# Kernel tuning notes

Measured on AMD Instinct MI355X. Metric: run time of the kernel, lower is better.

## Reference

```python
import jax, jax.numpy as jnp
import numpy as np

D_MODEL = 1024
EXPAND = 2
D_INNER = D_MODEL * EXPAND  # 2048
D_CONV = 4
B, T = 4, 4096
LN_EPS = 1e-5


def setup_inputs() -> dict:
    key = jax.random.key(0)
    ks = jax.random.split(key, 6)
    x = jax.random.normal(ks[0], (B, T, D_MODEL), dtype=jnp.float32)
    gamma = jnp.ones((D_MODEL,), jnp.float32)
    beta = jnp.zeros((D_MODEL,), jnp.float32)
    # in_proj: Linear(d_model -> 2*d_inner, bias=False); torch weight [out,in]
    W_in = jax.random.normal(ks[1], (2 * D_INNER, D_MODEL), jnp.float32) / np.sqrt(D_MODEL)
    # depthwise conv1d: weight [d_inner, 1, d_conv], bias [d_inner]
    conv_w = jax.random.normal(ks[2], (D_INNER, 1, D_CONV), jnp.float32) / np.sqrt(D_CONV)
    conv_b = jax.random.normal(ks[3], (D_INNER,), jnp.float32) * 0.01
    # out_proj: Linear(d_inner -> d_model, bias=False)
    W_out = jax.random.normal(ks[4], (D_MODEL, D_INNER), jnp.float32) / np.sqrt(D_INNER)
    return {"x": x, "gamma": gamma, "beta": beta, "W_in": W_in,
            "conv_w": conv_w, "conv_b": conv_b, "W_out": W_out}


def _silu(v):
    return v * jax.nn.sigmoid(v)


def reference(x, gamma, beta, W_in, conv_w, conv_b, W_out):
    residual = x
    # LayerNorm
    mu = jnp.mean(x, axis=-1, keepdims=True)
    var = jnp.mean(jnp.square(x - mu), axis=-1, keepdims=True)
    xn = (x - mu) * jax.lax.rsqrt(var + LN_EPS) * gamma + beta
    # in_proj -> split gate
    xz = jnp.einsum('btd,ed->bte', xn, W_in)  # [B,T,2*D_INNER]
    x_part, z = jnp.split(xz, 2, axis=-1)
    # causal depthwise conv: torch pads both sides by d_conv-1 then slices [:T]
    # == left pad (d_conv-1), no right pad
    lhs = jnp.transpose(x_part, (0, 2, 1))  # [B, D_INNER, T]
    x_conv = jax.lax.conv_general_dilated(
        lhs, conv_w, window_strides=(1,), padding=[(D_CONV - 1, 0)],
        feature_group_count=D_INNER,
        dimension_numbers=('NCH', 'OIH', 'NCH')) + conv_b[None, :, None]
    x_conv = jnp.transpose(x_conv, (0, 2, 1))  # [B,T,D_INNER]
    y = _silu(x_conv) * _silu(z)
    out = jnp.einsum('bte,de->btd', y, W_out)
    return residual + out  # dropout=0 (eval) -> identity
```

## Files before the change

### kernel.cpp

```cpp
#include <hip/hip_runtime.h>
#include <hip/hip_bf16.h>

#define D_MODEL 1024
#define D_INNER 2048
#define NTOK    16384
#define TLEN    4096
#define LN_EPS  1e-5f

typedef unsigned short u16;
typedef unsigned short u16x4 __attribute__((ext_vector_type(4)));
typedef unsigned short u16x8 __attribute__((ext_vector_type(8)));
typedef __bf16        bf16x8 __attribute__((ext_vector_type(8)));
typedef float         f32x4  __attribute__((ext_vector_type(4)));

__device__ __forceinline__ float b2f(u16 u) {
    union { float f; unsigned int i; } v; v.i = ((unsigned int)u) << 16; return v.f;
}
__device__ __forceinline__ u16 f2b(float f) {
    union { float f; unsigned int i; } v; v.f = f;
    unsigned int r = v.i + 0x7fffu + ((v.i >> 16) & 1u);
    return (u16)(r >> 16);
}

__device__ __forceinline__ void gld_lds16(const u16* g, u16* l) {
    __builtin_amdgcn_global_load_lds(
        (const __attribute__((address_space(1))) void*)g,
        (__attribute__((address_space(3))) void*)l, 16, 0, 0);
}

__device__ __forceinline__ void ln_body(
    int row, int tid,
    const float* __restrict__ x, const float* __restrict__ gamma,
    const float* __restrict__ beta, u16* __restrict__ xn)
{
    const float* xr = x + (size_t)row * D_MODEL;
    const int c0 = tid * 4;

    f32x4 xv = *(const f32x4*)(xr + c0);
    float s = 0.f, s2 = 0.f;
#pragma unroll
    for (int i = 0; i < 4; i++) { s += xv[i]; s2 += xv[i] * xv[i]; }

#pragma unroll
    for (int off = 32; off > 0; off >>= 1) {
        s  += __shfl_down(s,  off);
        s2 += __shfl_down(s2, off);
    }
    __shared__ float red[8];
    const int wave = tid >> 6, lane = tid & 63;
    if (lane == 0) { red[wave] = s; red[4 + wave] = s2; }
    __syncthreads();
    const float ts  = red[0] + red[1] + red[2] + red[3];
    const float ts2 = red[4] + red[5] + red[6] + red[7];
    const float mu  = ts * (1.0f / D_MODEL);
    const float var = ts2 * (1.0f / D_MODEL) - mu * mu;
    const float inv = rsqrtf(var + LN_EPS);

    f32x4 gv = *(const f32x4*)(gamma + c0);
    f32x4 bv = *(const f32x4*)(beta + c0);
    u16x4 out;
#pragma unroll
    for (int i = 0; i < 4; i++)
        out[i] = f2b((xv[i] - mu) * inv * gv[i] + bv[i]);
    *(u16x4*)(xn + (size_t)row * D_MODEL + c0) = out;
}

__global__ __launch_bounds__(256) void prep_kernel(
    const float* __restrict__ x, const float* __restrict__ gamma,
    const float* __restrict__ beta, u16* __restrict__ xn,
    const float* __restrict__ W_in, u16* __restrict__ wbin,
    const float* __restrict__ W_out, u16* __restrict__ wbout,
    const float* __restrict__ conv_w, float* __restrict__ wt,
    int lnRows)
{
    const int b   = blockIdx.x;
    const int tid = threadIdx.x;

    if (b < lnRows) {
        ln_body(b, tid, x, gamma, beta, xn);
        return;
    }
    int rb = b - lnRows;
    if (rb < 4096) {
        const int o = (rb * 256 + tid) * 4;
        f32x4 v = *(const f32x4*)(W_in + o);
        u16x4 w;
#pragma unroll
        for (int j = 0; j < 4; j++) w[j] = f2b(v[j]);
        *(u16x4*)(wbin + o) = w;
        return;
    }
    rb -= 4096;
    if (rb < 2048) {
        const int o = (rb * 256 + tid) * 4;
        f32x4 v = *(const f32x4*)(W_out + o);
        u16x4 w;
#pragma unroll
        for (int j = 0; j < 4; j++) w[j] = f2b(v[j]);
        *(u16x4*)(wbout + o) = w;
        return;
    }
    rb -= 2048;
    const int i = rb * 256 + tid;
    const int ch = i >> 2, j = i & 3;
    wt[j * D_INNER + ch] = conv_w[i];
}

__global__ __launch_bounds__(256) void ln_kernel(
    const float* __restrict__ x, const float* __restrict__ gamma,
    const float* __restrict__ beta, u16* __restrict__ xn)
{
    ln_body(blockIdx.x, threadIdx.x, x, gamma, beta, xn);
}

#define BAR()      __builtin_amdgcn_s_barrier()
#define WAIT_VM6() asm volatile("s_waitcnt vmcnt(6)" ::: "memory")
#define WAIT_VM0() asm volatile("s_waitcnt vmcnt(0)" ::: "memory")

#define STAGE_A(ldsb, s0, s1, kt) do { \
    gld_lds16(Ag + (size_t)(s0) * K + (kt) + goff, &(ldsb)[(s0) * 64]); \
    gld_lds16(Ag + (size_t)(s1) * K + (kt) + goff, &(ldsb)[(s1) * 64]); \
} while (0)
#define STAGE_B(ldsb, s0, s1, kt) do { \
    gld_lds16(Bg + (size_t)(s0) * K + (kt) + goff, &(ldsb)[(s0) * 64]); \
    gld_lds16(Bg + (size_t)(s1) * K + (kt) + goff, &(ldsb)[(s1) * 64]); \
} while (0)

#define RD_A(base, roff) do { \
    _Pragma("unroll") for (int m_ = 0; m_ < 4; m_++) { \
        const u16* p_ = (base) + (arow0 + (roff) + m_ * 16) * 64; \
        aF[m_][0] = __builtin_bit_cast(bf16x8, *(const u16x8*)(p_ + cx0)); \
        aF[m_][1] = __builtin_bit_cast(bf16x8, *(const u16x8*)(p_ + cx1)); \
    } } while (0)
#define RD_B(base, dst, roff) do { \
    _Pragma("unroll") for (int n_ = 0; n_ < 2; n_++) { \
        const u16* p_ = (base) + (brow0 + (roff) + n_ * 16) * 64; \
        dst[n_][0] = __builtin_bit_cast(bf16x8, *(const u16x8*)(p_ + cx0)); \
        dst[n_][1] = __builtin_bit_cast(bf16x8, *(const u16x8*)(p_ + cx1)); \
    } } while (0)

#define MMA_Q(m0, n0, BB) do { \
    _Pragma("unroll") for (int m_ = 0; m_ < 4; m_++) \
    _Pragma("unroll") for (int n_ = 0; n_ < 2; n_++) \
    _Pragma("unroll") for (int k_ = 0; k_ < 2; k_++) \
        acc[(m0) + m_][(n0) + n_] = __builtin_amdgcn_mfma_f32_16x16x32_bf16( \
            aF[m_][k_], BB[n_][k_], acc[(m0) + m_][(n0) + n_], 0, 0, 0); \
} while (0)

template<bool OUT_F32>
__global__ __launch_bounds__(512, 2) void gemm256(
    const u16* __restrict__ A, const u16* __restrict__ Bt,
    void* __restrict__ Cv, const float* __restrict__ Res,
    int M, int N, int K)
{
    __shared__ u16 As[2][256 * 64];
    __shared__ u16 Bs[2][256 * 64];

    const int tid  = threadIdx.x;
    const int wave = tid >> 6;
    const int lane = tid & 63;
    const int wm = wave >> 2, wn = wave & 3;
    const int lane15 = lane & 15, quad = lane >> 4;

    const int gx   = gridDim.x;
    const int nwg  = gx * gridDim.y;
    const int flat = blockIdx.y * gx + blockIdx.x;
    const int q8   = nwg >> 3;
    const int swz  = (flat & 7) * q8 + (flat >> 3);
    const int bm = swz % gx, bn = swz / gx;

    const u16* Ag = A  + (size_t)bm * 256 * K;
    const u16* Bg = Bt + (size_t)bn * 256 * K;

    const int lrow = lane >> 3;
    const int lcol = ((lane & 7) ^ lrow) * 8;
    const size_t goff = (size_t)lrow * K + lcol;

    const int aEv0 = wave * 8,      aEv1 = 128 + wave * 8;
    const int aOd0 = 64 + wave * 8, aOd1 = 192 + wave * 8;
    const int bEv0 = (wave >> 2) * 64 + (wave & 3) * 8, bEv1 = 128 + bEv0;
    const int bOd0 = bEv0 + 32,     bOd1 = bEv1 + 32;

    const int arow0 = wm * 128 + lane15;
    const int brow0 = wn * 64  + lane15;
    const int sw8   = lane15 & 7;
    const int cx0   = ((quad ^ sw8) << 3);
    const int cx1   = cx0 ^ 32;

    f32x4  acc[8][4] = {};
    bf16x8 aF[4][2], bE[2][2], bO[2][2];

    const int NT = K >> 6;
    const int NI = NT >> 1;

    STAGE_A(As[0], aEv0, aEv1, 0);
    STAGE_B(Bs[0], bEv0, bEv1, 0);
    STAGE_B(Bs[0], bOd0, bOd1, 0);
    STAGE_A(As[0], aOd0, aOd1, 0);
    STAGE_A(As[1], aEv0, aEv1, 64);
    STAGE_B(Bs[1], bEv0, bEv1, 64);
    STAGE_B(Bs[1], bOd0, bOd1, 64);
    WAIT_VM6();
    BAR();

    for (int i = 0; i < NI; i++) {
        const int kt0   = i * 128;
        const bool more = (i + 1 < NI);
#pragma unroll
        for (int h = 0; h < 2; h++) {
            const u16* as = As[h];
            const u16* bs = Bs[h];
            const int ktA = kt0 + 64  + h * 64;
            const int ktS = kt0 + 128 + h * 64;
            const bool gA = (h == 0) || more;
            const bool gS = more;

            RD_B(bs, bE, 0);
            RD_A(as, 0);
            if (gA) STAGE_A(As[h ^ 1], aOd0, aOd1, ktA);
            BAR();
            __builtin_amdgcn_s_setprio(1);
            MMA_Q(0, 0, bE);
            __builtin_amdgcn_s_setprio(0);
            BAR();

            RD_B(bs, bO, 32);
            if (gS) STAGE_A(As[h], aEv0, aEv1, ktS);
            BAR();
            __builtin_amdgcn_s_setprio(1);
            MMA_Q(0, 2, bO);
            __builtin_amdgcn_s_setprio(0);
            BAR();

            if (!more && h == 1) WAIT_VM0();
            RD_A(as, 64);
            if (gS) STAGE_B(Bs[h], bEv0, bEv1, ktS);
            BAR();
            __builtin_amdgcn_s_setprio(1);
            MMA_Q(4, 0, bE);
            __builtin_amdgcn_s_setprio(0);
            BAR();

            if (gS) STAGE_B(Bs[h], bOd0, bOd1, ktS);
            BAR();
            __builtin_amdgcn_s_setprio(1);
            MMA_Q(4, 2, bO);
            __builtin_amdgcn_s_setprio(0);
            if (more) WAIT_VM6();
            BAR();
        }
    }

    const int m0 = bm * 256 + wm * 128 + quad * 4;
    const int n0 = bn * 256 + wn * 64 + lane15;
#pragma unroll
    for (int mf = 0; mf < 8; mf++) {
#pragma unroll
        for (int nf = 0; nf < 4; nf++) {
#pragma unroll
            for (int i = 0; i < 4; i++) {
                const int r  = m0 + mf * 16 + i;
                const int cc = n0 + nf * 16;
                const size_t idx = (size_t)r * N + cc;
                float v = acc[mf][nf][i];
                if (OUT_F32) {
                    ((float*)Cv)[idx] = v + Res[idx];
                } else {
                    ((u16*)Cv)[idx] = f2b(v);
                }
            }
        }
    }
}

__global__ __launch_bounds__(256) void conv_gate8(
    const u16* __restrict__ xz, const float* __restrict__ wt,
    const float* __restrict__ conv_b, u16* __restrict__ y)
{
    const int tid  = threadIdx.x;
    const int row0 = blockIdx.x * 8;
    const int c    = tid * 8;
    const int t0   = row0 & (TLEN - 1);

    float w[4][8];
#pragma unroll
    for (int j = 0; j < 4; j++) {
        f32x4 a = *(const f32x4*)(wt + j * D_INNER + c);
        f32x4 b = *(const f32x4*)(wt + j * D_INNER + c + 4);
#pragma unroll
        for (int u = 0; u < 4; u++) { w[j][u] = a[u]; w[j][4 + u] = b[u]; }
    }
    float bias[8];
    {
        f32x4 a = *(const f32x4*)(conv_b + c);
        f32x4 b = *(const f32x4*)(conv_b + c + 4);
#pragma unroll
        for (int u = 0; u < 4; u++) { bias[u] = a[u]; bias[4 + u] = b[u]; }
    }

    u16x8 xv[11];
    if (t0 != 0) {
#pragma unroll
        for (int k = 0; k < 3; k++)
            xv[k] = *(const u16x8*)(xz + (size_t)(row0 - 3 + k) * 4096 + c);
    } else {
#pragma unroll
        for (int k = 0; k < 3; k++) xv[k] = (u16x8)0;
    }
#pragma unroll
    for (int k = 3; k < 11; k++)
        xv[k] = *(const u16x8*)(xz + (size_t)(row0 - 3 + k) * 4096 + c);

#pragma unroll
    for (int i = 0; i < 8; i++) {
        float acc[8];
#pragma unroll
        for (int u = 0; u < 8; u++) acc[u] = bias[u];
#pragma unroll
        for (int j = 0; j < 4; j++)
#pragma unroll
            for (int u = 0; u < 8; u++)
                acc[u] += b2f(xv[i + j][u]) * w[j][u];

        u16x8 zv = *(const u16x8*)(xz + (size_t)(row0 + i) * 4096 + 2048 + c);
        u16x8 out;
#pragma unroll
        for (int u = 0; u < 8; u++) {
            const float a = acc[u];
            const float z = b2f(zv[u]);
            const float sa = a / (1.0f + __expf(-a));
            const float sz = z / (1.0f + __expf(-z));
            out[u] = f2b(sa * sz);
        }
        *(u16x8*)(y + (size_t)(row0 + i) * (size_t)D_INNER + c) = out;
    }
}

extern "C" void kernel_launch(void* const* d_in, const int* in_sizes, int n_in,
                              void* d_out, int out_size, void* d_ws, size_t ws_size,
                              hipStream_t stream)
{
    const float* x      = (const float*)d_in[0];
    const float* gamma  = (const float*)d_in[1];
    const float* beta   = (const float*)d_in[2];
    const float* W_in   = (const float*)d_in[3];
    const float* conv_w = (const float*)d_in[4];
    const float* conv_b = (const float*)d_in[5];
    const float* W_out  = (const float*)d_in[6];
    float* out = (float*)d_out;

    const int nWin  = 4096 * 1024;
    const int nWout = 1024 * 2048;
    const int nWc   = D_INNER * 4;

    u16*   wbin  = (u16*)d_ws;
    u16*   wbout = wbin + nWin;
    float* wt    = (float*)(wbout + nWout);
    u16*   base  = (u16*)(wt + nWc);

    const size_t wbytes = (size_t)(nWin + nWout) * sizeof(u16) + nWc * sizeof(float);
    const size_t perRow = (size_t)(D_MODEL + 4096 + D_INNER) * sizeof(u16);
    int NC = 4;
    if (ws_size >= wbytes + (size_t)NTOK * perRow)          NC = 1;
    else if (ws_size >= wbytes + (size_t)(NTOK/2) * perRow) NC = 2;
    const int RC = NTOK / NC;

    u16* xn = base;
    u16* xz = xn + (size_t)RC * D_MODEL;
    u16* y  = xz + (size_t)RC * 4096;

    const int lnRows = (NC == 1) ? NTOK : 0;
    prep_kernel<<<lnRows + 4096 + 2048 + 32, 256, 0, stream>>>(
        x, gamma, beta, xn, W_in, wbin, W_out, wbout, conv_w, wt, lnRows);

    for (int c = 0; c < NC; c++) {
        const float* xc   = x   + (size_t)c * RC * D_MODEL;
        float*       outc = out + (size_t)c * RC * D_MODEL;

        if (NC > 1)
            ln_kernel<<<RC, 256, 0, stream>>>(xc, gamma, beta, xn);

        dim3 g1(RC / 256, (2 * D_INNER) / 256);
        gemm256<false><<<g1, 512, 0, stream>>>(xn, wbin, xz, nullptr,
                                               RC, 2 * D_INNER, D_MODEL);

        conv_gate8<<<RC / 8, 256, 0, stream>>>(xz, wt, conv_b, y);

        dim3 g2(RC / 256, D_MODEL / 256);
        gemm256<true><<<g2, 512, 0, stream>>>(y, wbout, outc, xc,
                                              RC, D_MODEL, D_INNER);
    }
}
```

Baseline: 400.9 us.

## Restructure GEMM main loop to prefetch LDS fragments across k-tiles

Reorganizes the double-buffered GEMM inner loop so that register fragments for the next sub-step (B odd half, A second half, and the next tile's A/B first halves) are read from LDS while the current MFMA block executes. Global-to-LDS staging of both A and B halves is regrouped after the MFMAs, with vmcnt waits changed to 8/4/0. The goal is to hide LDS read latency behind matrix ops. The cost is more live fragment registers, and the new barrier and wait placement must still keep buffer reuse free of races.

```diff
diff --git a/kernel.cpp b/kernel.cpp
--- a/kernel.cpp
+++ b/kernel.cpp
@@ -114,7 +114,8 @@
 }
 
 #define BAR()      __builtin_amdgcn_s_barrier()
-#define WAIT_VM6() asm volatile("s_waitcnt vmcnt(6)" ::: "memory")
+#define WAIT_VM8() asm volatile("s_waitcnt vmcnt(8)" ::: "memory")
+#define WAIT_VM4() asm volatile("s_waitcnt vmcnt(4)" ::: "memory")
 #define WAIT_VM0() asm volatile("s_waitcnt vmcnt(0)" ::: "memory")
 
 #define STAGE_A(ldsb, s0, s1, kt) do { \
@@ -140,11 +141,13 @@
     } } while (0)
 
 #define MMA_Q(m0, n0, BB) do { \
+    __builtin_amdgcn_s_setprio(1); \
     _Pragma("unroll") for (int m_ = 0; m_ < 4; m_++) \
     _Pragma("unroll") for (int n_ = 0; n_ < 2; n_++) \
     _Pragma("unroll") for (int k_ = 0; k_ < 2; k_++) \
         acc[(m0) + m_][(n0) + n_] = __builtin_amdgcn_mfma_f32_16x16x32_bf16( \
             aF[m_][k_], BB[n_][k_], acc[(m0) + m_][(n0) + n_], 0, 0, 0); \
+    __builtin_amdgcn_s_setprio(0); \
 } while (0)
 
 template<bool OUT_F32>
@@ -188,66 +191,56 @@
     const int cx1   = cx0 ^ 32;
 
     f32x4  acc[8][4] = {};
-    bf16x8 aF[4][2], bE[2][2], bO[2][2];
+    bf16x8 aF[4][2], bX[2][2], bY[2][2];
 
     const int NT = K >> 6;
     const int NI = NT >> 1;
 
     STAGE_A(As[0], aEv0, aEv1, 0);
     STAGE_B(Bs[0], bEv0, bEv1, 0);
+    STAGE_A(As[0], aOd0, aOd1, 0);
     STAGE_B(Bs[0], bOd0, bOd1, 0);
-    STAGE_A(As[0], aOd0, aOd1, 0);
     STAGE_A(As[1], aEv0, aEv1, 64);
     STAGE_B(Bs[1], bEv0, bEv1, 64);
+    STAGE_A(As[1], aOd0, aOd1, 64);
     STAGE_B(Bs[1], bOd0, bOd1, 64);
-    WAIT_VM6();
+    WAIT_VM0();
     BAR();
+    RD_A(As[0], 0);
+    RD_B(Bs[0], bX, 0);
 
     for (int i = 0; i < NI; i++) {
-        const int kt0   = i * 128;
         const bool more = (i + 1 < NI);
 #pragma unroll
         for (int h = 0; h < 2; h++) {
-            const u16* as = As[h];
-            const u16* bs = Bs[h];
-            const int ktA = kt0 + 64  + h * 64;
-            const int ktS = kt0 + 128 + h * 64;
-            const bool gA = (h == 0) || more;
-            const bool gS = more;
-
-            RD_B(bs, bE, 0);
-            RD_A(as, 0);
-            if (gA) STAGE_A(As[h ^ 1], aOd0, aOd1, ktA);
+            u16* as  = As[h];
+            u16* bs  = Bs[h];
+            const u16* asn = As[h ^ 1];
+            const u16* bsn = Bs[h ^ 1];
+            const int ktS  = i * 128 + 128 + h * 64;
+            const bool gN  = (h == 0) || more;
+            const bool gS  = more;
+            const bool lastT = (h == 1) && !more;
+
+            if (lastT) WAIT_VM0(); else WAIT_VM8();
             BAR();
-            __builtin_amdgcn_s_setprio(1);
-            MMA_Q(0, 0, bE);
-            __builtin_amdgcn_s_setprio(0);
+            RD_B(bs, bY, 32);
+            MMA_Q(0, 0, bX);
+
             BAR();
-
-            RD_B(bs, bO, 32);
-            if (gS) STAGE_A(As[h], aEv0, aEv1, ktS);
+            MMA_Q(0, 2, bY);
+            RD_A(as, 64);
+
+            if (!lastT) WAIT_VM4();
             BAR();
-            __builtin_amdgcn_s_setprio(1);
-            MMA_Q(0, 2, bO);
-            __builtin_amdgcn_s_setprio(0);
+            MMA_Q(4, 0, bX);
+            if (gN) RD_B(bsn, bX, 0);
+            if (gS) { STAGE_A(as, aEv0, aEv1, ktS); STAGE_B(bs, bEv0, bEv1, ktS); }
+
             BAR();
-
-            if (!more && h == 1) WAIT_VM0();
-            RD_A(as, 64);
-            if (gS) STAGE_B(Bs[h], bEv0, bEv1, ktS);
-            BAR();
-            __builtin_amdgcn_s_setprio(1);
-            MMA_Q(4, 0, bE);
-            __builtin_amdgcn_s_setprio(0);
-            BAR();
-
-            if (gS) STAGE_B(Bs[h], bOd0, bOd1, ktS);
-            BAR();
-            __builtin_amdgcn_s_setprio(1);
-            MMA_Q(4, 2, bO);
-            __builtin_amdgcn_s_setprio(0);
-            if (more) WAIT_VM6();
-            BAR();
+            MMA_Q(4, 2, bY);
+            if (gN) RD_A(asn, 0);
+            if (gS) { STAGE_A(as, aOd0, aOd1, ktS); STAGE_B(bs, bOd0, bOd1, ktS); }
         }
     }
 
```

Result: faster. 389.6 us (-2.8%).
